# Kernel optimization log

Hardware: AMD Instinct MI355X
Metric: run time of the kernel (lower is better)

Reference implementation:

```python
import jax, jax.numpy as jnp
import numpy as np

D, H, L, B = 32, 1024, 2, 4096


def _masks(d, h):
    # Sequential (natural) ordering degrees, as in MADE.create_masks
    d_in = jnp.arange(d)                      # input degrees
    d_hid = jnp.arange(h) % (d - 1)           # hidden degrees
    d_out = jnp.arange(d) % d - 1             # output degrees (= arange(d)-1)
    m0 = (d_hid[:, None] >= d_in[None, :]).astype(jnp.float32)   # [H, D]
    mh = (d_hid[:, None] >= d_hid[None, :]).astype(jnp.float32)  # [H, H]
    mo = (d_out[:, None] >= d_hid[None, :]).astype(jnp.float32)  # [D, H]
    mo = jnp.concatenate([mo, mo], axis=0)                       # [2D, H] (mask.repeat(2,1))
    return m0, mh, mo


def setup_inputs() -> dict:
    key = jax.random.key(0)
    ks = jax.random.split(key, 7)
    u = lambda k, shape, fan_in: jax.random.uniform(
        k, shape, minval=-1.0 / np.sqrt(fan_in), maxval=1.0 / np.sqrt(fan_in), dtype=jnp.float32)
    return {
        "z": jax.random.normal(ks[0], (B, D), dtype=jnp.float32),
        "W0": u(ks[1], (H, D), D),
        "b0": u(ks[2], (H,), D),
        "Wh": u(ks[3], (L, H, H), H),
        "bh": u(ks[4], (L, H), H),
        "Wout": u(ks[5], (2 * D, H), H),
        "bout": u(ks[6], (2 * D,), H),
    }


def reference(z, W0, b0, Wh, bh, Wout, bout):
    d = z.shape[1]
    h = W0.shape[0]
    m0, mh, mo = _masks(d, h)
    MW0 = m0 * W0                 # [H, D]
    MWh = mh[None, :, :] * Wh     # [L, H, H]
    MWo = mo * Wout               # [2D, H]

    def net(x):  # masked MLP: [B, D] -> [B, 2D]
        a = jax.nn.relu(x @ MW0.T + b0)
        for i in range(MWh.shape[0]):  # small fixed layer count
            a = jax.nn.relu(a @ MWh[i].T + bh[i])
        return a @ MWo.T + bout

    def step(x, idx):
        theta = net(x)  # [B, 2D]
        mu = jax.lax.dynamic_slice_in_dim(theta, idx, 1, axis=1)[:, 0]
        log_std = jax.lax.dynamic_slice_in_dim(theta, idx + d, 1, axis=1)[:, 0]
        zi = jax.lax.dynamic_slice_in_dim(z, idx, 1, axis=1)[:, 0]
        xi = zi * jnp.exp(log_std) + mu
        x = jax.lax.dynamic_update_slice(x, xi[:, None], (0, idx))
        return x, None

    x0 = jnp.zeros_like(z)
    x, _ = jax.lax.scan(step, x0, jnp.arange(d, dtype=jnp.int32))
    return x
```

## Files before the change

### kernel.cpp

```cpp
#include <hip/hip_runtime.h>
#include <hip/hip_bf16.h>

#define B_ 4096
#define D_ 32
#define H_ 1024
#define CS 512
#define WPK_L 1079296

typedef __attribute__((ext_vector_type(8))) short short8;
typedef __attribute__((ext_vector_type(4))) float floatx4;

#define BAR() __asm__ __volatile__("s_waitcnt lgkmcnt(0)\n\ts_barrier" ::: "memory")

__device__ inline unsigned short f2bf(float f) {
    unsigned u = __float_as_uint(f);
    unsigned r = (u + 0x7FFF + ((u >> 16) & 1)) >> 16;
    return (unsigned short)r;
}
__device__ inline void glds16(const void* g, void* l) {
    __builtin_amdgcn_global_load_lds(
        (const __attribute__((address_space(1))) unsigned int*)g,
        (__attribute__((address_space(3))) unsigned int*)l, 16, 0, 0);
}

__device__ inline int degs(int hp) { return (hp < 34) ? 0 : (hp - 1) / 33; }
__device__ inline int permf(int hp) {
    int d = degs(hp);
    int r = d ? (hp - 33 * d - 1) : hp;
    return d + 31 * r;
}
__device__ inline int band0i(int idx) {
    int nb0 = (idx == 1) ? 0 : 33 * idx - 32;
    return (nb0 > H_ - 64) ? H_ - 64 : nb0;
}

__global__ __launch_bounds__(256) void prep_all(
        const float* __restrict__ Wh, const float* __restrict__ W0,
        const float* __restrict__ Wout, const float* __restrict__ b0,
        const float* __restrict__ bh,
        unsigned short* __restrict__ Wpk, unsigned short* __restrict__ W0pk,
        unsigned short* __restrict__ Wopk, float* __restrict__ b0p,
        float* __restrict__ bhp) {
    __shared__ float row[H_];
    __shared__ unsigned short rb[H_];
    int b = blockIdx.x, t = threadIdx.x;
    if (b < 2048) {
        int l = b >> 10, np = b & 1023;
        const float* src = Wh + ((size_t)l << 20) + ((size_t)permf(np) << 10);
        ((float4*)row)[t] = ((const float4*)src)[t];
        __syncthreads();
        int dn = degs(np);
        unsigned short o[4];
        #pragma unroll
        for (int j = 0; j < 4; j++) {
            int kp = t * 4 + j;
            o[j] = (dn >= degs(kp)) ? f2bf(row[permf(kp)]) : (unsigned short)0;
        }
        ((ushort4*)rb)[t] = ushort4{o[0], o[1], o[2], o[3]};
        __syncthreads();
        for (int idx = 1; idx < 32; idx++) {
            int nb0 = band0i(idx);
            int j = np - nb0;
            if (j < 0 || j >= 64) continue;
            int nq = (idx + 1) * 4;
            if (t < nq) {
                int c = t >> 2, qd = t & 3;
                size_t base = (size_t)l * WPK_L + (size_t)1024 * (idx - 1) * (idx + 2);
                *(uint4*)(Wpk + base + c * 2048 + j * 32 + qd * 8) =
                    *(const uint4*)(rb + c * 32 + qd * 8);
            }
        }
    } else if (b < 2079) {
        int idx = b - 2047;
        int nb0 = band0i(idx);
        int j = t >> 2, ko = (t & 3) * 8;
        int n = nb0 + j;
        int dn = degs(n);
        const float* srow = W0 + (size_t)permf(n) * 32;
        union { unsigned short o[8]; uint4 v; } u;
        #pragma unroll
        for (int e = 0; e < 8; e++)
            u.o[e] = (dn >= ko + e) ? f2bf(srow[ko + e]) : (unsigned short)0;
        *(uint4*)(W0pk + (idx - 1) * 2048 + j * 32 + ko) = u.v;
    } else if (b < 3103) {
        int bb = b - 2079;
        int idx = bb >> 5, c = bb & 31;
        int ns = idx ? 33 * idx + 1 : 0;
        #pragma unroll
        for (int uu = 0; uu < 2; uu++) {
            int e = t + uu * 256;
            int col = e >> 5, k = e & 31;
            int h = c * 32 + k;
            unsigned short v = 0;
            if (col < 2 && h < ns)
                v = f2bf(Wout[(size_t)(idx + col * 32) * H_ + permf(h)]);
            Wopk[(size_t)bb * 512 + e] = v;
        }
    } else {
        int tt = (b - 3103) * 256 + t;
        int hp = tt & 1023;
        int p = permf(hp);
        if (tt < 1024) b0p[hp] = b0[p];
        else if (tt < 2048) bhp[hp] = bh[p];
        else bhp[1024 + hp] = bh[1024 + p];
    }
}

__device__ inline floatx4 mfma16(short8 a, short8 b, floatx4 c) {
    return __builtin_amdgcn_mfma_f32_16x16x32_bf16(a, b, c, 0, 0, 0);
}

__device__ inline floatx4 band_partial(const unsigned short* act, const unsigned short* wpk,
                                       int frow, int fk, int s, int c0, int c1) {
    const unsigned short* ap = act + frow * 32 + fk * 8;
    const unsigned short* wp = wpk + s * 512 + frow * 32 + fk * 8;
    floatx4 x = {0.f, 0.f, 0.f, 0.f}, y = {0.f, 0.f, 0.f, 0.f};
    int c = c0;
    for (; c + 1 < c1; c += 2) {
        short8 a0 = *(const short8*)(ap + c * CS);
        short8 b0 = *(const short8*)(wp + (size_t)c * 2048);
        short8 a1 = *(const short8*)(ap + (c + 1) * CS);
        short8 b1 = *(const short8*)(wp + (size_t)(c + 1) * 2048);
        x = mfma16(a0, b0, x);
        y = mfma16(a1, b1, y);
    }
    if (c < c1) {
        short8 a0 = *(const short8*)(ap + c * CS);
        short8 b0 = *(const short8*)(wp + (size_t)c * 2048);
        x = mfma16(a0, b0, x);
    }
    return x + y;
}

__global__ __launch_bounds__(1024) void mega_kernel(
        const float* __restrict__ z,
        const unsigned short* __restrict__ W0pk,
        const float* __restrict__ b0p,
        const unsigned short* __restrict__ Wpk,
        const float* __restrict__ bhp,
        const unsigned short* __restrict__ Wopk,
        const float* __restrict__ bout,
        float* __restrict__ xout) {
    __shared__ unsigned short aS[3 * 32 * CS];
    __shared__ unsigned short xbS[16 * 32];
    __shared__ float xsS[512];
    __shared__ float zsS[512];
    __shared__ floatx4 redS[12 * 64];
    __shared__ float redO[16 * 32];
    __shared__ uint4 dummyS[64];

    const int tid = threadIdx.x;
    const int wave = tid >> 6, lane = tid & 63;
    const int frow = lane & 15, fk = lane >> 4;
    const int arow = frow * 32 + fk * 8;
    const int s = wave & 3, q = wave >> 2;
    const int m0 = blockIdx.x * 16;

    {
        uint4 zz = {0u, 0u, 0u, 0u};
        for (int i = tid; i < 3 * 32 * CS / 8; i += 1024) ((uint4*)aS)[i] = zz;
        if (tid < 64)  ((uint4*)xbS)[tid] = zz;
        if (tid < 128) ((uint4*)xsS)[tid] = zz;
        if (tid < 128) ((uint4*)redO)[tid] = zz;
        if (tid < 128) ((float4*)zsS)[tid] = ((const float4*)(z + (size_t)m0 * 32))[tid];
    }
    __syncthreads();

    unsigned short* a1 = aS;
    unsigned short* a2 = aS + 32 * CS;
    unsigned short* a3 = aS + 64 * CS;

    for (int idx = 0; idx < 32; idx++) {
        if (idx > 0) {
            const int nb0 = band0i(idx);
            const int slot = nb0 + s * 16 + frow;
            const int nk = idx + 1;
            const int nk4 = (nk + 3) >> 2;
            const int c0 = q * nk4;
            const int c1m = (c0 + nk4 < nk) ? c0 + nk4 : nk;
            const unsigned short* wb2 = Wpk + (size_t)1024 * (idx - 1) * (idx + 2);
            const unsigned short* wb3 = wb2 + WPK_L;
            const int wsl = (slot >> 5) * CS + (slot & 31);

            if (q == 0) {
                short8 a = *(const short8*)(xbS + frow * 32 + fk * 8);
                short8 bf = *(const short8*)(W0pk + (idx - 1) * 2048 + (s * 16 + frow) * 32 + fk * 8);
                floatx4 acc = {0.f, 0.f, 0.f, 0.f};
                acc = mfma16(a, bf, acc);
                float bb = b0p[slot];
                #pragma unroll
                for (int r = 0; r < 4; r++)
                    a1[wsl + (fk * 4 + r) * 32] = f2bf(fmaxf(acc[r] + bb, 0.f));
            }
            BAR();

            {
                floatx4 p = band_partial(a1, wb2, frow, fk, s, c0, c1m);
                if (q) redS[((q - 1) * 4 + s) * 64 + lane] = p;
                BAR();
                if (q == 0) {
                    p = p + redS[s * 64 + lane] + redS[(4 + s) * 64 + lane]
                          + redS[(8 + s) * 64 + lane];
                    float bb = bhp[slot];
                    #pragma unroll
                    for (int r = 0; r < 4; r++)
                        a2[wsl + (fk * 4 + r) * 32] = f2bf(fmaxf(p[r] + bb, 0.f));
                }
                BAR();
            }

            {
                floatx4 g = band_partial(a2, wb3, frow, fk, s, c0, c1m);
                if (q) redS[((q - 1) * 4 + s) * 64 + lane] = g;
                BAR();
                if (q == 0) {
                    g = g + redS[s * 64 + lane] + redS[(4 + s) * 64 + lane]
                          + redS[(8 + s) * 64 + lane];
                    float bb = bhp[H_ + slot];
                    #pragma unroll
                    for (int r = 0; r < 4; r++)
                        a3[wsl + (fk * 4 + r) * 32] = f2bf(fmaxf(g[r] + bb, 0.f));
                }
                BAR();
            }
        }

        {
            floatx4 oacc = {0.f, 0.f, 0.f, 0.f};
            #pragma unroll
            for (int cc = 0; cc < 2; cc++) {
                int c = wave * 2 + cc;
                short8 a = *(const short8*)(a3 + c * CS + arow);
                short8 bf = *(const short8*)(Wopk + (size_t)((idx * 32 + c) * 16 + frow) * 32 + fk * 8);
                oacc = mfma16(a, bf, oacc);
            }
            if (frow < 2) {
                #pragma unroll
                for (int r = 0; r < 4; r++)
                    redO[wave * 32 + frow * 16 + fk * 4 + r] = oacc[r];
            }
        }

        if (idx < 31) {
            const int slice = (blockIdx.x >> 3) & 31;
            const char* w2n = (const char*)(Wpk + (size_t)1024 * idx * (idx + 3));
            const char* w3n = w2n + (size_t)WPK_L * 2;
            const int bytesn = (idx + 2) * 4096;
            const char* won = (const char*)(Wopk + (size_t)(idx + 1) * 32 * 512);
            int off = (slice & 7) * 16384;
            if (off < bytesn) {
                glds16(w2n + off + tid * 16, dummyS);
                glds16(w3n + off + tid * 16, dummyS);
            }
            glds16(won + (slice & 1) * 16384 + tid * 16, dummyS);
        }
        BAR();

        if (tid < 16) {
            float sm = bout[idx], sl = bout[idx + D_];
            #pragma unroll
            for (int w = 0; w < 16; w++) {
                sm += redO[w * 32 + tid];
                sl += redO[w * 32 + 16 + tid];
            }
            float xi = fmaf(zsS[tid * 32 + idx], expf(sl), sm);
            xsS[tid * 32 + idx] = xi;
            xbS[tid * 32 + idx] = f2bf(xi);
        }
        BAR();
    }

    __syncthreads();
    if (tid < 128)
        ((float4*)(xout + (size_t)m0 * 32))[tid] = ((const float4*)xsS)[tid];
}

extern "C" void kernel_launch(void* const* d_in, const int* in_sizes, int n_in,
                              void* d_out, int out_size, void* d_ws, size_t ws_size,
                              hipStream_t stream) {
    const float* z    = (const float*)d_in[0];
    const float* W0   = (const float*)d_in[1];
    const float* b0   = (const float*)d_in[2];
    const float* Wh   = (const float*)d_in[3];
    const float* bh   = (const float*)d_in[4];
    const float* Wout = (const float*)d_in[5];
    const float* bout = (const float*)d_in[6];

    float* x = (float*)d_out;
    unsigned short* Wpk  = (unsigned short*)d_ws;
    unsigned short* W0pk = Wpk + 2 * WPK_L;
    unsigned short* Wopk = W0pk + 31 * 2048;
    float* b0p = (float*)(Wopk + 32 * 32 * 512);
    float* bhp = b0p + H_;

    prep_all<<<3115, 256, 0, stream>>>(Wh, W0, Wout, b0, bh, Wpk, W0pk, Wopk, b0p, bhp);

    mega_kernel<<<B_ / 16, 1024, 0, stream>>>(z, W0pk, b0p, Wpk, bhp, Wopk, bout, x);
}
```

Baseline: 218.4 us.

## Software-prefetch next layer weights into registers instead of L2 warming

Replaces the global_load_lds L2-warming prefetch with explicit register prefetch of the next band's weight fragments, biases and output weights, issued right after the current layer's MFMAs so the loads overlap barriers and reductions. The band loop is unrolled up to eight chunks using the register-held operands. The final per-step reduction is split across a full wave using shuffles, and z is transposed in shared memory to avoid strided reads. This uses more VGPRs per thread at 1024 threads per block, which could cause spills.

Result: faster. 196.7 us (-9.9%).

```diff
diff --git a/kernel.cpp b/kernel.cpp
--- a/kernel.cpp
+++ b/kernel.cpp
@@ -16,11 +16,6 @@
     unsigned u = __float_as_uint(f);
     unsigned r = (u + 0x7FFF + ((u >> 16) & 1)) >> 16;
     return (unsigned short)r;
-}
-__device__ inline void glds16(const void* g, void* l) {
-    __builtin_amdgcn_global_load_lds(
-        (const __attribute__((address_space(1))) unsigned int*)g,
-        (__attribute__((address_space(3))) unsigned int*)l, 16, 0, 0);
 }
 
 __device__ inline int degs(int hp) { return (hp < 34) ? 0 : (hp - 1) / 33; }
@@ -110,27 +105,19 @@
     return __builtin_amdgcn_mfma_f32_16x16x32_bf16(a, b, c, 0, 0, 0);
 }
 
-__device__ inline floatx4 band_partial(const unsigned short* act, const unsigned short* wpk,
-                                       int frow, int fk, int s, int c0, int c1) {
-    const unsigned short* ap = act + frow * 32 + fk * 8;
-    const unsigned short* wp = wpk + s * 512 + frow * 32 + fk * 8;
-    floatx4 x = {0.f, 0.f, 0.f, 0.f}, y = {0.f, 0.f, 0.f, 0.f};
-    int c = c0;
-    for (; c + 1 < c1; c += 2) {
-        short8 a0 = *(const short8*)(ap + c * CS);
-        short8 b0 = *(const short8*)(wp + (size_t)c * 2048);
-        short8 a1 = *(const short8*)(ap + (c + 1) * CS);
-        short8 b1 = *(const short8*)(wp + (size_t)(c + 1) * 2048);
-        x = mfma16(a0, b0, x);
-        y = mfma16(a1, b1, y);
-    }
-    if (c < c1) {
-        short8 a0 = *(const short8*)(ap + c * CS);
-        short8 b0 = *(const short8*)(wp + (size_t)c * 2048);
-        x = mfma16(a0, b0, x);
-    }
-    return x + y;
-}
+#define BAND_PARTIAL(act, outv) do {                                          \
+    const unsigned short* ap_ = (act) + arow;                                 \
+    floatx4 x_ = {0.f, 0.f, 0.f, 0.f}, y_ = {0.f, 0.f, 0.f, 0.f};             \
+    _Pragma("unroll")                                                         \
+    for (int j_ = 0; j_ < 8; j_++) {                                          \
+        if (j_ < nch) {                                                       \
+            short8 a_ = *(const short8*)(ap_ + (size_t)(c0 + j_) * CS);       \
+            if (j_ & 1) y_ = mfma16(a_, rb[j_], y_);                          \
+            else        x_ = mfma16(a_, rb[j_], x_);                          \
+        }                                                                     \
+    }                                                                         \
+    outv = x_ + y_;                                                           \
+} while (0)
 
 __global__ __launch_bounds__(1024) void mega_kernel(
         const float* __restrict__ z,
@@ -144,10 +131,9 @@
     __shared__ unsigned short aS[3 * 32 * CS];
     __shared__ unsigned short xbS[16 * 32];
     __shared__ float xsS[512];
-    __shared__ float zsS[512];
+    __shared__ float zsT[512];
     __shared__ floatx4 redS[12 * 64];
     __shared__ float redO[16 * 32];
-    __shared__ uint4 dummyS[64];
 
     const int tid = threadIdx.x;
     const int wave = tid >> 6, lane = tid & 63;
@@ -162,13 +148,63 @@
         if (tid < 64)  ((uint4*)xbS)[tid] = zz;
         if (tid < 128) ((uint4*)xsS)[tid] = zz;
         if (tid < 128) ((uint4*)redO)[tid] = zz;
-        if (tid < 128) ((float4*)zsS)[tid] = ((const float4*)(z + (size_t)m0 * 32))[tid];
+        if (tid < 128) {
+            float4 v = ((const float4*)(z + (size_t)m0 * 32))[tid];
+            int row = tid >> 3, c4 = (tid & 7) * 4;
+            zsT[(c4 + 0) * 16 + row] = v.x;
+            zsT[(c4 + 1) * 16 + row] = v.y;
+            zsT[(c4 + 2) * 16 + row] = v.z;
+            zsT[(c4 + 3) * 16 + row] = v.w;
+        }
     }
     __syncthreads();
 
     unsigned short* a1 = aS;
     unsigned short* a2 = aS + 32 * CS;
     unsigned short* a3 = aS + 64 * CS;
+
+    short8 rb[8];
+    short8 rbf;
+    short8 rwo0, rwo1;
+    float pb0 = 0.f, pb2 = 0.f, pb3 = 0.f;
+    float pbo_m = 0.f, pbo_s = 0.f;
+
+    rwo0 = *(const short8*)(Wopk + (size_t)((wave * 2) * 16 + frow) * 32 + fk * 8);
+    rwo1 = *(const short8*)(Wopk + (size_t)((wave * 2 + 1) * 16 + frow) * 32 + fk * 8);
+    if (wave == 0) { pbo_m = bout[0]; pbo_s = bout[D_]; }
+
+    auto pfL2 = [&](int nidx) {
+        const int nkn = nidx + 1;
+        const int nk4n = (nkn + 3) >> 2;
+        const int c0n = q * nk4n;
+        const int c1n = (c0n + nk4n < nkn) ? c0n + nk4n : nkn;
+        const int nchn = c1n - c0n;
+        const unsigned short* w2 = Wpk + (size_t)1024 * (nidx - 1) * (nidx + 2)
+                                 + s * 512 + frow * 32 + fk * 8;
+        #pragma unroll
+        for (int j = 0; j < 8; j++)
+            if (j < nchn) rb[j] = *(const short8*)(w2 + (size_t)(c0n + j) * 2048);
+        if (q == 0) {
+            const int nb0n = band0i(nidx);
+            const int slotn = nb0n + s * 16 + frow;
+            rbf = *(const short8*)(W0pk + (nidx - 1) * 2048 + (s * 16 + frow) * 32 + fk * 8);
+            pb0 = b0p[slotn];
+            pb2 = bhp[slotn];
+            pb3 = bhp[H_ + slotn];
+        }
+    };
+    auto pfL3 = [&](int cidx) {
+        const int nkn = cidx + 1;
+        const int nk4n = (nkn + 3) >> 2;
+        const int c0n = q * nk4n;
+        const int c1n = (c0n + nk4n < nkn) ? c0n + nk4n : nkn;
+        const int nchn = c1n - c0n;
+        const unsigned short* w3 = Wpk + WPK_L + (size_t)1024 * (cidx - 1) * (cidx + 2)
+                                 + s * 512 + frow * 32 + fk * 8;
+        #pragma unroll
+        for (int j = 0; j < 8; j++)
+            if (j < nchn) rb[j] = *(const short8*)(w3 + (size_t)(c0n + j) * 2048);
+    };
 
     for (int idx = 0; idx < 32; idx++) {
         if (idx > 0) {
@@ -178,61 +214,67 @@
             const int nk4 = (nk + 3) >> 2;
             const int c0 = q * nk4;
             const int c1m = (c0 + nk4 < nk) ? c0 + nk4 : nk;
-            const unsigned short* wb2 = Wpk + (size_t)1024 * (idx - 1) * (idx + 2);
-            const unsigned short* wb3 = wb2 + WPK_L;
+            const int nch = c1m - c0;
             const int wsl = (slot >> 5) * CS + (slot & 31);
+            const float pb3c = pb3;
 
             if (q == 0) {
-                short8 a = *(const short8*)(xbS + frow * 32 + fk * 8);
-                short8 bf = *(const short8*)(W0pk + (idx - 1) * 2048 + (s * 16 + frow) * 32 + fk * 8);
+                short8 a = *(const short8*)(xbS + arow);
                 floatx4 acc = {0.f, 0.f, 0.f, 0.f};
-                acc = mfma16(a, bf, acc);
-                float bb = b0p[slot];
+                acc = mfma16(a, rbf, acc);
                 #pragma unroll
                 for (int r = 0; r < 4; r++)
-                    a1[wsl + (fk * 4 + r) * 32] = f2bf(fmaxf(acc[r] + bb, 0.f));
+                    a1[wsl + (fk * 4 + r) * 32] = f2bf(fmaxf(acc[r] + pb0, 0.f));
             }
             BAR();
 
             {
-                floatx4 p = band_partial(a1, wb2, frow, fk, s, c0, c1m);
+                floatx4 p;
+                BAND_PARTIAL(a1, p);
+                pfL3(idx);
                 if (q) redS[((q - 1) * 4 + s) * 64 + lane] = p;
                 BAR();
                 if (q == 0) {
                     p = p + redS[s * 64 + lane] + redS[(4 + s) * 64 + lane]
                           + redS[(8 + s) * 64 + lane];
-                    float bb = bhp[slot];
                     #pragma unroll
                     for (int r = 0; r < 4; r++)
-                        a2[wsl + (fk * 4 + r) * 32] = f2bf(fmaxf(p[r] + bb, 0.f));
+                        a2[wsl + (fk * 4 + r) * 32] = f2bf(fmaxf(p[r] + pb2, 0.f));
                 }
                 BAR();
             }
 
             {
-                floatx4 g = band_partial(a2, wb3, frow, fk, s, c0, c1m);
+                floatx4 g;
+                BAND_PARTIAL(a2, g);
+                if (idx < 31) pfL2(idx + 1);
                 if (q) redS[((q - 1) * 4 + s) * 64 + lane] = g;
                 BAR();
                 if (q == 0) {
                     g = g + redS[s * 64 + lane] + redS[(4 + s) * 64 + lane]
                           + redS[(8 + s) * 64 + lane];
-                    float bb = bhp[H_ + slot];
                     #pragma unroll
                     for (int r = 0; r < 4; r++)
-                        a3[wsl + (fk * 4 + r) * 32] = f2bf(fmaxf(g[r] + bb, 0.f));
+                        a3[wsl + (fk * 4 + r) * 32] = f2bf(fmaxf(g[r] + pb3c, 0.f));
                 }
                 BAR();
             }
-        }
+        } else {
+            pfL2(1);
+        }
+
+        const float bm = pbo_m, bs = pbo_s;
 
         {
             floatx4 oacc = {0.f, 0.f, 0.f, 0.f};
-            #pragma unroll
-            for (int cc = 0; cc < 2; cc++) {
-                int c = wave * 2 + cc;
-                short8 a = *(const short8*)(a3 + c * CS + arow);
-                short8 bf = *(const short8*)(Wopk + (size_t)((idx * 32 + c) * 16 + frow) * 32 + fk * 8);
-                oacc = mfma16(a, bf, oacc);
+            short8 av0 = *(const short8*)(a3 + (wave * 2) * CS + arow);
+            short8 av1 = *(const short8*)(a3 + (wave * 2 + 1) * CS + arow);
+            oacc = mfma16(av0, rwo0, oacc);
+            oacc = mfma16(av1, rwo1, oacc);
+            if (idx < 31) {
+                rwo0 = *(const short8*)(Wopk + (size_t)(((idx + 1) * 32 + wave * 2) * 16 + frow) * 32 + fk * 8);
+                rwo1 = *(const short8*)(Wopk + (size_t)(((idx + 1) * 32 + wave * 2 + 1) * 16 + frow) * 32 + fk * 8);
+                if (wave == 0) { pbo_m = bout[idx + 1]; pbo_s = bout[idx + 1 + D_]; }
             }
             if (frow < 2) {
                 #pragma unroll
@@ -240,32 +282,21 @@
                     redO[wave * 32 + frow * 16 + fk * 4 + r] = oacc[r];
             }
         }
-
-        if (idx < 31) {
-            const int slice = (blockIdx.x >> 3) & 31;
-            const char* w2n = (const char*)(Wpk + (size_t)1024 * idx * (idx + 3));
-            const char* w3n = w2n + (size_t)WPK_L * 2;
-            const int bytesn = (idx + 2) * 4096;
-            const char* won = (const char*)(Wopk + (size_t)(idx + 1) * 32 * 512);
-            int off = (slice & 7) * 16384;
-            if (off < bytesn) {
-                glds16(w2n + off + tid * 16, dummyS);
-                glds16(w3n + off + tid * 16, dummyS);
-            }
-            glds16(won + (slice & 1) * 16384 + tid * 16, dummyS);
-        }
         BAR();
 
-        if (tid < 16) {
-            float sm = bout[idx], sl = bout[idx + D_];
+        if (wave == 0) {
+            const int col = lane & 31;
+            const int wbase = (lane >> 5) * 8;
+            float v = 0.f;
             #pragma unroll
-            for (int w = 0; w < 16; w++) {
-                sm += redO[w * 32 + tid];
-                sl += redO[w * 32 + 16 + tid];
-            }
-            float xi = fmaf(zsS[tid * 32 + idx], expf(sl), sm);
-            xsS[tid * 32 + idx] = xi;
-            xbS[tid * 32 + idx] = f2bf(xi);
+            for (int w = 0; w < 8; w++) v += redO[(wbase + w) * 32 + col];
+            v += __shfl_xor(v, 32);
+            float vs = __shfl(v, (lane & 15) + 16);
+            if (lane < 16) {
+                float xi = fmaf(zsT[idx * 16 + lane], expf(bs + vs), bm + v);
+                xsS[lane * 32 + idx] = xi;
+                xbS[lane * 32 + idx] = f2bf(xi);
+            }
         }
         BAR();
     }
```

## Warp-specialize mega kernel into critical-path wave and pipelined partial-sum waves

Applied to the files above, without the earlier changes.

Replaces the uniform per-step layer sweep with warp specialization. Wave 0 computes only the newly exposed band columns of each layer on the critical path. Waves 1-8, 9-12 and 13-15 precompute partial sums for layer 2, layer 3 and the output layer for the next step from already-final activations, with weights preloaded into registers. Partial sums are double-buffered in LDS, and the L2 prefetch via global_load_lds is removed. The aim is to shorten the serial dependency chain per autoregressive step and overlap weight loads. In exchange it adds many register arrays, a delicate barrier count that must match across roles, and the risk of load imbalance.

Result: slower. 275.1 us (+26.0%).

```diff
diff --git a/kernel.cpp b/kernel.cpp
--- a/kernel.cpp
+++ b/kernel.cpp
@@ -16,11 +16,6 @@
     unsigned u = __float_as_uint(f);
     unsigned r = (u + 0x7FFF + ((u >> 16) & 1)) >> 16;
     return (unsigned short)r;
-}
-__device__ inline void glds16(const void* g, void* l) {
-    __builtin_amdgcn_global_load_lds(
-        (const __attribute__((address_space(1))) unsigned int*)g,
-        (__attribute__((address_space(3))) unsigned int*)l, 16, 0, 0);
 }
 
 __device__ inline int degs(int hp) { return (hp < 34) ? 0 : (hp - 1) / 33; }
@@ -110,27 +105,20 @@
     return __builtin_amdgcn_mfma_f32_16x16x32_bf16(a, b, c, 0, 0, 0);
 }
 
-__device__ inline floatx4 band_partial(const unsigned short* act, const unsigned short* wpk,
-                                       int frow, int fk, int s, int c0, int c1) {
-    const unsigned short* ap = act + frow * 32 + fk * 8;
-    const unsigned short* wp = wpk + s * 512 + frow * 32 + fk * 8;
-    floatx4 x = {0.f, 0.f, 0.f, 0.f}, y = {0.f, 0.f, 0.f, 0.f};
-    int c = c0;
-    for (; c + 1 < c1; c += 2) {
-        short8 a0 = *(const short8*)(ap + c * CS);
-        short8 b0 = *(const short8*)(wp + (size_t)c * 2048);
-        short8 a1 = *(const short8*)(ap + (c + 1) * CS);
-        short8 b1 = *(const short8*)(wp + (size_t)(c + 1) * 2048);
-        x = mfma16(a0, b0, x);
-        y = mfma16(a1, b1, y);
+#define PIECE(MAXJ, lo, hi, act, base_c)                                        \
+    _Pragma("unroll")                                                           \
+    for (int j_ = 0; j_ < (MAXJ); ++j_) {                                       \
+        if (j_ >= (lo) && j_ < (hi)) {                                          \
+            short8 a_ = *(const short8*)((act) + (size_t)((base_c) + j_) * CS + arow); \
+            if (j_ & 1) aB = mfma16(a_, rb[j_], aB);                            \
+            else        aA = mfma16(a_, rb[j_], aA);                            \
+        }                                                                       \
     }
-    if (c < c1) {
-        short8 a0 = *(const short8*)(ap + c * CS);
-        short8 b0 = *(const short8*)(wp + (size_t)c * 2048);
-        x = mfma16(a0, b0, x);
-    }
-    return x + y;
-}
+
+#define LOADW(MAXJ, cnt, wp, stride)                                            \
+    _Pragma("unroll")                                                           \
+    for (int j_ = 0; j_ < (MAXJ); ++j_)                                         \
+        if (j_ < (cnt)) rb[j_] = *(const short8*)((wp) + (size_t)j_ * (stride));
 
 __global__ __launch_bounds__(1024) void mega_kernel(
         const float* __restrict__ z,
@@ -142,27 +130,38 @@
         const float* __restrict__ bout,
         float* __restrict__ xout) {
     __shared__ unsigned short aS[3 * 32 * CS];
-    __shared__ unsigned short xbS[16 * 32];
+    __shared__ unsigned short xbS[512];
     __shared__ float xsS[512];
-    __shared__ float zsS[512];
-    __shared__ floatx4 redS[12 * 64];
-    __shared__ float redO[16 * 32];
-    __shared__ uint4 dummyS[64];
+    __shared__ float zsT[512];
+    __shared__ floatx4 redS2[2 * 8 * 64];
+    __shared__ floatx4 redS3[2 * 4 * 64];
+    __shared__ floatx4 redO[2 * 3 * 64];
 
     const int tid = threadIdx.x;
     const int wave = tid >> 6, lane = tid & 63;
     const int frow = lane & 15, fk = lane >> 4;
     const int arow = frow * 32 + fk * 8;
-    const int s = wave & 3, q = wave >> 2;
     const int m0 = blockIdx.x * 16;
+    const floatx4 FZ = {0.f, 0.f, 0.f, 0.f};
 
     {
         uint4 zz = {0u, 0u, 0u, 0u};
         for (int i = tid; i < 3 * 32 * CS / 8; i += 1024) ((uint4*)aS)[i] = zz;
         if (tid < 64)  ((uint4*)xbS)[tid] = zz;
         if (tid < 128) ((uint4*)xsS)[tid] = zz;
-        if (tid < 128) ((uint4*)redO)[tid] = zz;
-        if (tid < 128) ((float4*)zsS)[tid] = ((const float4*)(z + (size_t)m0 * 32))[tid];
+        for (int i = tid; i < 1920; i += 1024) {
+            if (i < 1024)      ((uint4*)redS2)[i] = zz;
+            else if (i < 1536) ((uint4*)redS3)[i - 1024] = zz;
+            else               ((uint4*)redO)[i - 1536] = zz;
+        }
+        if (tid < 128) {
+            float4 v = ((const float4*)(z + (size_t)m0 * 32))[tid];
+            int row = tid >> 3, c4 = (tid & 7) * 4;
+            zsT[(c4 + 0) * 16 + row] = v.x;
+            zsT[(c4 + 1) * 16 + row] = v.y;
+            zsT[(c4 + 2) * 16 + row] = v.z;
+            zsT[(c4 + 3) * 16 + row] = v.w;
+        }
     }
     __syncthreads();
 
@@ -170,104 +169,198 @@
     unsigned short* a2 = aS + 32 * CS;
     unsigned short* a3 = aS + 64 * CS;
 
-    for (int idx = 0; idx < 32; idx++) {
-        if (idx > 0) {
+    if (wave == 0) {
+        __builtin_amdgcn_s_setprio(1);
+        short8 w0f[4], w2f[8], w3f[8], wof[2];
+        float b0v[4], b2v[4], b3v[4];
+        float bm = bout[0], bs = bout[D_];
+        #pragma unroll 1
+        for (int idx = 0; idx < 32; ++idx) {
             const int nb0 = band0i(idx);
-            const int slot = nb0 + s * 16 + frow;
-            const int nk = idx + 1;
-            const int nk4 = (nk + 3) >> 2;
-            const int c0 = q * nk4;
-            const int c1m = (c0 + nk4 < nk) ? c0 + nk4 : nk;
-            const unsigned short* wb2 = Wpk + (size_t)1024 * (idx - 1) * (idx + 2);
-            const unsigned short* wb3 = wb2 + WPK_L;
-            const int wsl = (slot >> 5) * CS + (slot & 31);
-
-            if (q == 0) {
-                short8 a = *(const short8*)(xbS + frow * 32 + fk * 8);
-                short8 bf = *(const short8*)(W0pk + (idx - 1) * 2048 + (s * 16 + frow) * 32 + fk * 8);
-                floatx4 acc = {0.f, 0.f, 0.f, 0.f};
-                acc = mfma16(a, bf, acc);
-                float bb = b0p[slot];
-                #pragma unroll
-                for (int r = 0; r < 4; r++)
-                    a1[wsl + (fk * 4 + r) * 32] = f2bf(fmaxf(acc[r] + bb, 0.f));
-            }
-            BAR();
-
+            const int cb0 = idx - 1;
+            if (idx > 0) {
+                short8 xa = *(const short8*)(xbS + arow);
+                #pragma unroll
+                for (int s2 = 0; s2 < 4; ++s2) {
+                    floatx4 acc = mfma16(xa, w0f[s2], FZ);
+                    const int slot = nb0 + s2 * 16 + frow;
+                    const int wsl = (slot >> 5) * CS + (slot & 31);
+                    #pragma unroll
+                    for (int r = 0; r < 4; ++r)
+                        a1[wsl + (fk * 4 + r) * 32] = f2bf(fmaxf(acc[r] + b0v[s2], 0.f));
+                }
+                const unsigned short* wp = Wpk + (size_t)1024 * (idx - 1) * (idx + 2)
+                                         + frow * 32 + fk * 8;
+                #pragma unroll
+                for (int s2 = 0; s2 < 4; ++s2) {
+                    w2f[s2 * 2 + 0] = *(const short8*)(wp + s2 * 512 + (size_t)(idx - 1) * 2048);
+                    w2f[s2 * 2 + 1] = *(const short8*)(wp + s2 * 512 + (size_t)idx * 2048);
+                    b2v[s2] = bhp[nb0 + s2 * 16 + frow];
+                }
+            }
+            BAR();
+            if (idx > 0) {
+                short8 af0 = *(const short8*)(a1 + (size_t)cb0 * CS + arow);
+                short8 af1 = *(const short8*)(a1 + (size_t)(cb0 + 1) * CS + arow);
+                #pragma unroll
+                for (int s2 = 0; s2 < 4; ++s2) {
+                    floatx4 acc = redS2[((idx & 1) * 8 + s2) * 64 + lane]
+                                + redS2[((idx & 1) * 8 + 4 + s2) * 64 + lane];
+                    acc = mfma16(af0, w2f[s2 * 2 + 0], acc);
+                    acc = mfma16(af1, w2f[s2 * 2 + 1], acc);
+                    const int slot = nb0 + s2 * 16 + frow;
+                    const int wsl = (slot >> 5) * CS + (slot & 31);
+                    #pragma unroll
+                    for (int r = 0; r < 4; ++r)
+                        a2[wsl + (fk * 4 + r) * 32] = f2bf(fmaxf(acc[r] + b2v[s2], 0.f));
+                }
+                const unsigned short* wp = Wpk + WPK_L + (size_t)1024 * (idx - 1) * (idx + 2)
+                                         + frow * 32 + fk * 8;
+                #pragma unroll
+                for (int s2 = 0; s2 < 4; ++s2) {
+                    w3f[s2 * 2 + 0] = *(const short8*)(wp + s2 * 512 + (size_t)(idx - 1) * 2048);
+                    w3f[s2 * 2 + 1] = *(const short8*)(wp + s2 * 512 + (size_t)idx * 2048);
+                    b3v[s2] = bhp[H_ + nb0 + s2 * 16 + frow];
+                }
+            }
+            BAR();
+            if (idx > 0) {
+                short8 af0 = *(const short8*)(a2 + (size_t)cb0 * CS + arow);
+                short8 af1 = *(const short8*)(a2 + (size_t)(cb0 + 1) * CS + arow);
+                #pragma unroll
+                for (int s2 = 0; s2 < 4; ++s2) {
+                    floatx4 acc = redS3[((idx & 1) * 4 + s2) * 64 + lane];
+                    acc = mfma16(af0, w3f[s2 * 2 + 0], acc);
+                    acc = mfma16(af1, w3f[s2 * 2 + 1], acc);
+                    const int slot = nb0 + s2 * 16 + frow;
+                    const int wsl = (slot >> 5) * CS + (slot & 31);
+                    #pragma unroll
+                    for (int r = 0; r < 4; ++r)
+                        a3[wsl + (fk * 4 + r) * 32] = f2bf(fmaxf(acc[r] + b3v[s2], 0.f));
+                }
+                #pragma unroll
+                for (int cc = 0; cc < 2; ++cc)
+                    wof[cc] = *(const short8*)(Wopk
+                        + (size_t)((idx * 32 + cb0 + cc) * 16 + frow) * 32 + fk * 8);
+            }
+            if (idx < 31) {
+                const int nbn = band0i(idx + 1);
+                #pragma unroll
+                for (int s2 = 0; s2 < 4; ++s2) {
+                    w0f[s2] = *(const short8*)(W0pk + idx * 2048 + (s2 * 16 + frow) * 32 + fk * 8);
+                    b0v[s2] = b0p[nbn + s2 * 16 + frow];
+                }
+            }
+            BAR();
             {
-                floatx4 p = band_partial(a1, wb2, frow, fk, s, c0, c1m);
-                if (q) redS[((q - 1) * 4 + s) * 64 + lane] = p;
-                BAR();
-                if (q == 0) {
-                    p = p + redS[s * 64 + lane] + redS[(4 + s) * 64 + lane]
-                          + redS[(8 + s) * 64 + lane];
-                    float bb = bhp[slot];
+                floatx4 od = redO[((idx & 1) * 3 + 0) * 64 + lane]
+                           + redO[((idx & 1) * 3 + 1) * 64 + lane]
+                           + redO[((idx & 1) * 3 + 2) * 64 + lane];
+                if (idx > 0) {
+                    short8 af0 = *(const short8*)(a3 + (size_t)cb0 * CS + arow);
+                    short8 af1 = *(const short8*)(a3 + (size_t)(cb0 + 1) * CS + arow);
+                    od = mfma16(af0, wof[0], od);
+                    od = mfma16(af1, wof[1], od);
+                }
+                float lsv[4];
+                #pragma unroll
+                for (int r = 0; r < 4; ++r)
+                    lsv[r] = __shfl(od[r], (lane & 48) + 1);
+                if (frow == 0) {
                     #pragma unroll
-                    for (int r = 0; r < 4; r++)
-                        a2[wsl + (fk * 4 + r) * 32] = f2bf(fmaxf(p[r] + bb, 0.f));
-                }
-                BAR();
-            }
-
+                    for (int r = 0; r < 4; ++r) {
+                        const int row = fk * 4 + r;
+                        float xi = fmaf(zsT[idx * 16 + row], expf(bs + lsv[r]), bm + od[r]);
+                        xsS[row * 32 + idx] = xi;
+                        xbS[row * 32 + idx] = f2bf(xi);
+                    }
+                }
+                if (idx < 31) { bm = bout[idx + 1]; bs = bout[idx + 1 + D_]; }
+            }
+        }
+    } else if (wave <= 8) {
+        const int s2w = (wave - 1) & 3, h2 = (wave - 1) >> 2;
+        short8 rb[15];
+        floatx4 aA = FZ, aB = FZ;
+        int cl = 0, cnt = 0, p = 0, p2 = 0;
+        #pragma unroll 1
+        for (int idx = 0; idx < 32; ++idx) {
+            BAR();
+            PIECE(15, 0, p, a1, cl);
+            BAR();
+            PIECE(15, p, p2, a1, cl);
+            BAR();
+            PIECE(15, p2, cnt, a1, cl);
+            if (idx < 31)
+                redS2[(((idx + 1) & 1) * 8 + h2 * 4 + s2w) * 64 + lane] = aA + aB;
+            if (idx < 30) {
+                const int cbn = idx + 1;
+                const int hc = (cbn + 1) >> 1;
+                cl = h2 ? hc : 0;
+                const int ch = h2 ? cbn : hc;
+                cnt = ch - cl;
+                p = (cnt + 2) / 3;
+                p2 = (2 * p < cnt) ? 2 * p : cnt;
+                const unsigned short* wp = Wpk + (size_t)1024 * (idx + 1) * (idx + 4)
+                                         + s2w * 512 + frow * 32 + fk * 8 + (size_t)cl * 2048;
+                LOADW(15, cnt, wp, 2048);
+                aA = FZ; aB = FZ;
+            } else { cnt = 0; p = 0; p2 = 0; }
+        }
+    } else if (wave <= 12) {
+        const int s3 = wave - 9;
+        short8 rb[15];
+        floatx4 aA = FZ, aB = FZ;
+        int cnt = 0, h = 0;
+        #pragma unroll 1
+        for (int idx = 0; idx < 32; ++idx) {
+            PIECE(15, 0, cnt - h, a2, h);
+            BAR();
+            if (idx >= 1)
+                redS3[((idx & 1) * 4 + s3) * 64 + lane] = aA + aB;
+            aA = FZ; aB = FZ;
             {
-                floatx4 g = band_partial(a2, wb3, frow, fk, s, c0, c1m);
-                if (q) redS[((q - 1) * 4 + s) * 64 + lane] = g;
-                BAR();
-                if (q == 0) {
-                    g = g + redS[s * 64 + lane] + redS[(4 + s) * 64 + lane]
-                          + redS[(8 + s) * 64 + lane];
-                    float bb = bhp[H_ + slot];
-                    #pragma unroll
-                    for (int r = 0; r < 4; r++)
-                        a3[wsl + (fk * 4 + r) * 32] = f2bf(fmaxf(g[r] + bb, 0.f));
-                }
-                BAR();
-            }
-        }
-
-        {
-            floatx4 oacc = {0.f, 0.f, 0.f, 0.f};
-            #pragma unroll
-            for (int cc = 0; cc < 2; cc++) {
-                int c = wave * 2 + cc;
-                short8 a = *(const short8*)(a3 + c * CS + arow);
-                short8 bf = *(const short8*)(Wopk + (size_t)((idx * 32 + c) * 16 + frow) * 32 + fk * 8);
-                oacc = mfma16(a, bf, oacc);
-            }
-            if (frow < 2) {
-                #pragma unroll
-                for (int r = 0; r < 4; r++)
-                    redO[wave * 32 + frow * 16 + fk * 4 + r] = oacc[r];
-            }
-        }
-
-        if (idx < 31) {
-            const int slice = (blockIdx.x >> 3) & 31;
-            const char* w2n = (const char*)(Wpk + (size_t)1024 * idx * (idx + 3));
-            const char* w3n = w2n + (size_t)WPK_L * 2;
-            const int bytesn = (idx + 2) * 4096;
-            const char* won = (const char*)(Wopk + (size_t)(idx + 1) * 32 * 512);
-            int off = (slice & 7) * 16384;
-            if (off < bytesn) {
-                glds16(w2n + off + tid * 16, dummyS);
-                glds16(w3n + off + tid * 16, dummyS);
-            }
-            glds16(won + (slice & 1) * 16384 + tid * 16, dummyS);
-        }
-        BAR();
-
-        if (tid < 16) {
-            float sm = bout[idx], sl = bout[idx + D_];
-            #pragma unroll
-            for (int w = 0; w < 16; w++) {
-                sm += redO[w * 32 + tid];
-                sl += redO[w * 32 + 16 + tid];
-            }
-            float xi = fmaf(zsS[tid * 32 + idx], expf(sl), sm);
-            xsS[tid * 32 + idx] = xi;
-            xbS[tid * 32 + idx] = f2bf(xi);
-        }
-        BAR();
+                cnt = (idx < 31) ? idx : 0;
+                h = (cnt + 1) >> 1;
+                const unsigned short* wp = Wpk + WPK_L + (size_t)1024 * idx * (idx + 3)
+                                         + s3 * 512 + frow * 32 + fk * 8;
+                LOADW(15, h, wp, 2048);
+            }
+            BAR();
+            PIECE(15, 0, h, a2, 0);
+            {
+                const unsigned short* wp = Wpk + WPK_L + (size_t)1024 * idx * (idx + 3)
+                                         + s3 * 512 + frow * 32 + fk * 8 + (size_t)h * 2048;
+                LOADW(15, cnt - h, wp, 2048);
+            }
+            BAR();
+        }
+    } else {
+        const int k3 = wave - 13;
+        short8 rb[10];
+        floatx4 aA = FZ, aB = FZ;
+        int cl = 0, cnt = 0;
+        #pragma unroll 1
+        for (int idx = 0; idx < 32; ++idx) {
+            BAR();
+            if (idx < 31) {
+                const int cbn = idx;
+                const int ot = (cbn + 2) / 3;
+                cl = k3 * ot;
+                int ch = cl + ot; if (ch > cbn) ch = cbn;
+                cnt = ch - cl; if (cnt < 0) cnt = 0;
+                const unsigned short* wp = Wopk
+                    + (size_t)(((idx + 1) * 32 + cl) * 16 + frow) * 32 + fk * 8;
+                LOADW(10, cnt, wp, 512);
+                aA = FZ; aB = FZ;
+            }
+            BAR();
+            BAR();
+            if (idx < 31) {
+                PIECE(10, 0, cnt, a3, cl);
+                redO[(((idx + 1) & 1) * 3 + k3) * 64 + lane] = aA + aB;
+            }
+        }
     }
 
     __syncthreads();
```
